# Performance work log

Hardware: AMD Instinct MI355X
Metric: run time of the kernel (lower is better)

The kernel has to match this reference:

```python
import jax, jax.numpy as jnp
import numpy as np

B, S, D, R = 4, 4096, 1024, 128
EPS_MAG = 1e-8
EPS_LN = 1e-5


def setup_inputs() -> dict:
    key = jax.random.key(0)
    ks = jax.random.split(key, 24)
    w = lambda k, shape, s=0.02: (jax.random.normal(k, shape, jnp.float32) * s)
    d = {}
    d["x"] = jax.random.normal(ks[0], (B, S, D), jnp.float32)
    d["W_dt_down"] = w(ks[1], (D, R))            # dt_proj_down (no bias)
    d["W_dt_up"] = w(ks[2], (R, D))
    d["b_dt_up"] = jnp.full((D,), -4.0, jnp.float32)  # nn.init.constant_(-4.0)
    d["W_gate"] = w(ks[3], (D, D)); d["b_gate"] = jnp.zeros((D,), jnp.float32)
    d["W_phi1"] = w(ks[4], (D, D)); d["b_phi1"] = jnp.zeros((D,), jnp.float32)
    d["W_phi2"] = w(ks[5], (D, D)); d["b_phi2"] = jnp.zeros((D,), jnp.float32)
    d["omega_base"] = jax.random.normal(ks[6], (D,), jnp.float32) * 0.1
    d["W_omega"] = w(ks[7], (D, D)); d["b_omega"] = jnp.zeros((D,), jnp.float32)
    d["W_mag"] = w(ks[8], (D, D)); d["b_mag"] = jnp.zeros((D,), jnp.float32)
    d["W_qoff"] = w(ks[9], (D, D)); d["b_qoff"] = jnp.zeros((D,), jnp.float32)
    d["ln_g"] = jnp.ones((2 * D,), jnp.float32); d["ln_b"] = jnp.zeros((2 * D,), jnp.float32)
    d["W_out1"] = w(ks[10], (2 * D, D)); d["b_out1"] = jnp.zeros((D,), jnp.float32)
    d["W_out2"] = w(ks[11], (D, D)); d["b_out2"] = jnp.zeros((D,), jnp.float32)
    return d


def _forward(x, W_dt_down, W_dt_up, b_dt_up, W_gate, b_gate, W_phi1, b_phi1,
             W_phi2, b_phi2, omega_base, W_omega, b_omega, W_mag, b_mag,
             W_qoff, b_qoff, ln_g, ln_b, W_out1, b_out1, W_out2, b_out2):
    h = x  # expand_factor == 1 -> in_proj is Identity
    # input-dependent delta (low-rank)
    dt = jax.nn.softplus((h @ W_dt_down) @ W_dt_up + b_dt_up)        # [B,S,D]
    select_gate = jax.nn.sigmoid(h @ W_gate + b_gate)
    omega = omega_base + (h @ W_omega + b_omega)
    omega_scaled = omega * dt * 0.01
    phi_init = jax.nn.gelu(h @ W_phi1 + b_phi1, approximate=False) @ W_phi2 + b_phi2
    phi = phi_init + jnp.cumsum(omega_scaled, axis=1)                # phase accumulation
    magnitude = jax.nn.sigmoid(h @ W_mag + b_mag) * 5.0
    content = select_gate * h * magnitude
    memory_real = jnp.cumsum(content * jnp.cos(phi), axis=1)
    memory_imag = jnp.cumsum(content * jnp.sin(phi), axis=1)
    acc_mag = jnp.cumsum(magnitude * select_gate, axis=1)
    sqrt_mag = jnp.sqrt(acc_mag + EPS_MAG)
    mr = memory_real / sqrt_mag
    mi = memory_imag / sqrt_mag
    # rotation-based retrieval
    phi_q = phi + (h @ W_qoff + b_qoff)
    cq, sq = jnp.cos(phi_q), jnp.sin(phi_q)
    retrieved_real = mr * cq + mi * sq
    retrieved_imag = mi * cq - mr * sq
    ctx = jnp.concatenate([retrieved_real, retrieved_imag], axis=-1)  # [B,S,2D]
    mu = jnp.mean(ctx, axis=-1, keepdims=True)
    var = jnp.mean((ctx - mu) ** 2, axis=-1, keepdims=True)
    ln = (ctx - mu) / jnp.sqrt(var + EPS_LN) * ln_g + ln_b
    out = jax.nn.gelu(ln @ W_out1 + b_out1, approximate=False) @ W_out2 + b_out2
    return x + out


def reference(x, W_dt_down, W_dt_up, b_dt_up, W_gate, b_gate, W_phi1, b_phi1,
              W_phi2, b_phi2, omega_base, W_omega, b_omega, W_mag, b_mag,
              W_qoff, b_qoff, ln_g, ln_b, W_out1, b_out1, W_out2, b_out2):
    return _forward(x, W_dt_down, W_dt_up, b_dt_up, W_gate, b_gate, W_phi1, b_phi1,
                    W_phi2, b_phi2, omega_base, W_omega, b_omega, W_mag, b_mag,
                    W_qoff, b_qoff, ln_g, ln_b, W_out1, b_out1, W_out2, b_out2)
```

## Files before the change

kernel.cpp:

```cpp
#include <hip/hip_runtime.h>


#define D_ 1024
#define S_ 4096
#define MQ 4096
#define MF 16384
#define CHUNK 64
#define NCH (S_/CHUNK)

typedef float f32x4 __attribute__((ext_vector_type(4)));
typedef __bf16 bf16x8 __attribute__((ext_vector_type(8)));
typedef short s16x8 __attribute__((ext_vector_type(8)));

typedef __attribute__((address_space(1))) void gvoid;
typedef __attribute__((address_space(3))) void lvoid;

__device__ __forceinline__ void g2l16(const void* g, void* l) {
  __builtin_amdgcn_global_load_lds((gvoid*)g, (lvoid*)l, 16, 0, 0);
}

__device__ __forceinline__ float bflo(unsigned int w){ union{unsigned int i; float f;} c; c.i = w<<16; return c.f; }
__device__ __forceinline__ float bfhi(unsigned int w){ union{unsigned int i; float f;} c; c.i = w & 0xFFFF0000u; return c.f; }
__device__ __forceinline__ unsigned short f2bf(float f){
  union{float f; unsigned int i;} c; c.f=f;
  unsigned int u = c.i + 0x7FFFu + ((c.i>>16)&1u);
  return (unsigned short)(u>>16);
}
__device__ __forceinline__ unsigned int pack2(float lo, float hi){
  return (unsigned int)f2bf(lo) | ((unsigned int)f2bf(hi)<<16);
}

__device__ __forceinline__ float sig_(float x){ return 1.f/(1.f+__expf(-x)); }
__device__ __forceinline__ float gelu_(float x){ return 0.5f*x*(1.f+erff(x*0.70710678118654752440f)); }
__device__ __forceinline__ float softplus_(float x){ return (x>0.f) ? x + log1pf(__expf(-x)) : log1pf(__expf(x)); }

template<int MODE>
__global__ __launch_bounds__(256)
void gemmF(const unsigned short* __restrict__ A0,
           const unsigned short* __restrict__ A1,
           const unsigned short* __restrict__ B0,
           const unsigned short* __restrict__ B1,
           const float* __restrict__ bias0,
           const float* __restrict__ bias1,
           const float* __restrict__ extra,
           unsigned short* __restrict__ out0,
           unsigned short* __restrict__ out1,
           float* __restrict__ outf)
{
  __shared__ unsigned short As[2][128*32];
  __shared__ unsigned short Bs[2][128*32];
  const int tid = threadIdx.x;
  const int m0 = blockIdx.x * 128;
  const int n0 = blockIdx.y * 128;
  const int lane = tid & 63;
  const int wv = tid >> 6;
  const int wr = wv >> 1, wc = wv & 1;
  const int fr = lane & 15, fg = lane >> 4;

  const int r0 = tid >> 2;
  const int r1 = (tid + 256) >> 2;
  const int k8 = (tid & 3) * 8;

  const unsigned short* Ap; const unsigned short* Bp;
  int lda, ldb, K, brow0;
  if constexpr (MODE == 0)      { Ap=A0; lda=1024; K=1024; Bp=B0; ldb=1024; brow0=n0; }
  else if constexpr (MODE == 2) { Ap=A0; lda=2048; K=2048; Bp=B0; ldb=2048; brow0=n0; }
  else if constexpr (MODE == 3) { Ap=A0; lda=1024; K=1024; Bp=B0; ldb=1024; brow0=n0; }
  else {
    if (n0 < 1024) { Ap=A0; lda=1024; K=1024; Bp=B0; ldb=1024; brow0=n0; }
    else           { Ap=A1; lda=128;  K=128;  Bp=B1; ldb=128;  brow0=n0-1024; }
  }

  const unsigned short* ArowA = Ap + (size_t)(m0+r0)*lda + k8;
  const unsigned short* ArowB = Ap + (size_t)(m0+r1)*lda + k8;
  const unsigned short* BrowA = Bp + (size_t)(brow0+r0)*ldb + k8;
  const unsigned short* BrowB = Bp + (size_t)(brow0+r1)*ldb + k8;

  f32x4 acc[4][4];
#pragma unroll
  for (int i=0;i<4;i++)
#pragma unroll
    for (int j=0;j<4;j++)
#pragma unroll
      for (int q=0;q<4;q++) acc[i][j][q] = 0.f;

  auto STAGE = [&](int buf, int t) {
    const int k0 = t << 5;
    g2l16(ArowA + k0, &As[buf][(size_t)tid*8]);
    g2l16(ArowB + k0, &As[buf][(size_t)(tid+256)*8]);
    g2l16(BrowA + k0, &Bs[buf][(size_t)tid*8]);
    g2l16(BrowB + k0, &Bs[buf][(size_t)(tid+256)*8]);
  };
  auto COMPUTE = [&](int buf) {
    s16x8 af[4], bfr[4];
#pragma unroll
    for (int mf=0; mf<4; mf++) af[mf]  = *(const s16x8*)&As[buf][(wr*64 + mf*16 + fr)*32 + fg*8];
#pragma unroll
    for (int nf=0; nf<4; nf++) bfr[nf] = *(const s16x8*)&Bs[buf][(wc*64 + nf*16 + fr)*32 + fg*8];
#pragma unroll
    for (int mf=0; mf<4; mf++)
#pragma unroll
      for (int nf=0; nf<4; nf++)
        acc[mf][nf] = __builtin_amdgcn_mfma_f32_16x16x32_bf16(
          __builtin_bit_cast(bf16x8, af[mf]), __builtin_bit_cast(bf16x8, bfr[nf]),
          acc[mf][nf], 0, 0, 0);
  };

  const int nt = K >> 5;
  STAGE(0, 0);
  STAGE(1, 1);
  int cur = 0;
  for (int t = 0; t < nt - 1; ++t) {
    asm volatile("s_waitcnt vmcnt(4)" ::: "memory");
    __builtin_amdgcn_s_barrier();
    __builtin_amdgcn_sched_barrier(0);
    COMPUTE(cur);
    __builtin_amdgcn_s_barrier();
    __builtin_amdgcn_sched_barrier(0);
    if (t + 2 < nt) STAGE(cur, t + 2);
    cur ^= 1;
  }
  asm volatile("s_waitcnt vmcnt(0)" ::: "memory");
  __builtin_amdgcn_s_barrier();
  __builtin_amdgcn_sched_barrier(0);
  COMPUTE(cur);

  const int slice = n0 >> 10;
#pragma unroll
  for (int mf=0; mf<4; mf++) {
#pragma unroll
    for (int nf=0; nf<4; nf++) {
      const int gn = n0 + wc*64 + nf*16 + fr;
      float bv;
      if constexpr (MODE == 1) bv = (n0 < 1024) ? bias0[gn] : bias1[gn-1024];
      else bv = bias0[gn];
#pragma unroll
      for (int q=0; q<4; q++) {
        const int gm = m0 + wr*64 + mf*16 + fg*4 + q;
        const float z = acc[mf][nf][q] + bv;
        if constexpr (MODE == 0) {
          if (slice < 5) {
            const float r = (slice==0) ? sig_(z)
                          : (slice==2) ? gelu_(z)
                          : (slice==3) ? sig_(z)*5.f : z;
            out0[(size_t)slice*MQ*1024 + (size_t)gm*1024 + (gn&1023)] = f2bf(r);
          } else {
            out1[(size_t)gm*128 + (gn-5120)] = f2bf(z);
          }
        } else if constexpr (MODE == 1) {
          if (slice == 0) out0[(size_t)gm*1024 + gn] = f2bf(z);
          else            out1[(size_t)gm*1024 + (gn-1024)] = f2bf(softplus_(z));
        } else if constexpr (MODE == 2) {
          out0[(size_t)gm*1024 + gn] = f2bf(gelu_(z));
        } else {
          const size_t idx = (size_t)gm*1024 + gn;
          outf[idx] = z + extra[idx];
        }
      }
    }
  }
}

__global__ __launch_bounds__(256)
void cvtx_k(const float* __restrict__ x, unsigned int* __restrict__ hb)
{
  const size_t i = (size_t)blockIdx.x*256 + threadIdx.x;
  const float4 v = *(const float4*)(x + i*4);
  hb[i*2]   = pack2(v.x, v.y);
  hb[i*2+1] = pack2(v.z, v.w);
}

__global__ __launch_bounds__(256)
void tconv_k(const float* __restrict__ W, unsigned short* __restrict__ Wt, int K, int N)
{
  __shared__ float tile[32][33];
  const int kb = blockIdx.x*32, nb = blockIdx.y*32;
  const int tx = threadIdx.x & 31, ty = threadIdx.x >> 5;
#pragma unroll
  for (int i=0;i<32;i+=8) tile[ty+i][tx] = W[(size_t)(kb+ty+i)*N + (nb+tx)];
  __syncthreads();
#pragma unroll
  for (int i=0;i<32;i+=8) Wt[(size_t)(nb+ty+i)*K + (kb+tx)] = f2bf(tile[tx][ty+i]);
}

struct P7 { const float* s[7]; unsigned short* d[7]; };
__global__ __launch_bounds__(256)
void tconv7_k(P7 p)
{
  __shared__ float tile[32][33];
  const float* W = p.s[blockIdx.z];
  unsigned short* Wt = p.d[blockIdx.z];
  const int kb = blockIdx.x*32, nb = blockIdx.y*32;
  const int tx = threadIdx.x & 31, ty = threadIdx.x >> 5;
#pragma unroll
  for (int i=0;i<32;i+=8) tile[ty+i][tx] = W[(size_t)(kb+ty+i)*1024 + (nb+tx)];
  __syncthreads();
#pragma unroll
  for (int i=0;i<32;i+=8) Wt[(size_t)(nb+ty+i)*1024 + (kb+tx)] = f2bf(tile[tx][ty+i]);
}

__global__ __launch_bounds__(256)
void biascat_k(const float* bg, const float* bo, const float* ob, const float* bp1,
               const float* bm, const float* bq, float* bc)
{
  const int i = blockIdx.x*256 + threadIdx.x;
  if (i >= 5248) return;
  const int s = i >> 10, d = i & 1023;
  float v;
  if (s==0) v = bg[d];
  else if (s==1) v = bo[d] + ob[d];
  else if (s==2) v = bp1[d];
  else if (s==3) v = bm[d];
  else if (s==4) v = bq[d];
  else v = 0.f;
  bc[i] = v;
}

__global__ __launch_bounds__(256)
void scan1_k(unsigned int* __restrict__ zgate, unsigned int* __restrict__ zmag,
             unsigned int* __restrict__ zomega, const unsigned int* __restrict__ zdt,
             const unsigned int* __restrict__ hb,
             float* __restrict__ sumPhi, float* __restrict__ sumGm)
{
  const int flat = blockIdx.x*256 + threadIdx.x;
  const int dh = flat & 511;
  const int bc = flat >> 9;
  size_t i = (size_t)bc*CHUNK*(D_/2) + dh;
  float sp0=0,sp1=0,sg0=0,sg1=0;
  for (int s=0;s<CHUNK;s++,i+=D_/2) {
    const unsigned ga=zgate[i], mg=zmag[i], om=zomega[i], dt=zdt[i], hh=hb[i];
    const float ga0=bflo(ga), ga1=bfhi(ga), mg0=bflo(mg), mg1=bfhi(mg);
    const float od0 = bflo(om)*bflo(dt)*0.01f, od1 = bfhi(om)*bfhi(dt)*0.01f;
    const unsigned odp = pack2(od0, od1);
    zomega[i] = odp;
    sp0 += bflo(odp); sp1 += bfhi(odp);
    const float g0 = ga0*mg0, g1 = ga1*mg1;
    const unsigned gmp = pack2(g0, g1);
    zmag[i] = gmp;
    sg0 += bflo(gmp); sg1 += bfhi(gmp);
    zgate[i] = pack2(g0*bflo(hh), g1*bfhi(hh));
  }
  const int sidx = bc*D_ + dh*2;
  sumPhi[sidx]=sp0; sumPhi[sidx+1]=sp1;
  sumGm[sidx]=sg0;  sumGm[sidx+1]=sg1;
}

__global__ __launch_bounds__(256)
void scan2_k(float* __restrict__ a, float* __restrict__ b)
{
  const int chain = (blockIdx.x*256 + threadIdx.x) >> 6;
  const int lane  = threadIdx.x & 63;
  const size_t i = (size_t)lane*D_ + chain;
  const float v = a[i], w = b[i];
  float vi = v, wi = w;
#pragma unroll
  for (int off=1; off<64; off<<=1) {
    const float t = __shfl_up(vi, off, 64);
    const float u = __shfl_up(wi, off, 64);
    if (lane >= off) { vi += t; wi += u; }
  }
  a[i] = vi - v;
  b[i] = wi - w;
}

__global__ __launch_bounds__(256)
void scan3_k(const unsigned int* __restrict__ omdt, const unsigned int* __restrict__ content,
             const unsigned int* __restrict__ phinit, const float* __restrict__ phiOff,
             float* __restrict__ sumRe, float* __restrict__ sumIm)
{
  const int flat = blockIdx.x*256 + threadIdx.x;
  const int dh = flat & 511;
  const int bc = flat >> 9;
  size_t i = (size_t)bc*CHUNK*(D_/2) + dh;
  const int sidx = bc*D_ + dh*2;
  float p0 = phiOff[sidx], p1 = phiOff[sidx+1];
  float re0=0,re1=0,im0=0,im1=0;
  for (int s=0;s<CHUNK;s++,i+=D_/2) {
    const unsigned od = omdt[i], ct = content[i], pi = phinit[i];
    p0 += bflo(od); p1 += bfhi(od);
    const float phi0 = bflo(pi)+p0, phi1 = bfhi(pi)+p1;
    float s0,c0,s1,c1;
    __sincosf(phi0,&s0,&c0);
    __sincosf(phi1,&s1,&c1);
    const float ct0=bflo(ct), ct1=bfhi(ct);
    re0 += ct0*c0; im0 += ct0*s0;
    re1 += ct1*c1; im1 += ct1*s1;
  }
  sumRe[sidx]=re0; sumRe[sidx+1]=re1;
  sumIm[sidx]=im0; sumIm[sidx+1]=im1;
}

__global__ __launch_bounds__(256)
void scan5_k(const unsigned int* __restrict__ omdt, const unsigned int* __restrict__ content,
             const unsigned int* __restrict__ phinit, const unsigned int* __restrict__ gm,
             const unsigned int* __restrict__ qoff,
             const float* __restrict__ phiOff, const float* __restrict__ gmOff,
             const float* __restrict__ reOff, const float* __restrict__ imOff,
             unsigned int* __restrict__ ctx)
{
  const int flat = blockIdx.x*256 + threadIdx.x;
  const int dh = flat & 511;
  const int bc = flat >> 9;
  size_t i = (size_t)bc*CHUNK*(D_/2) + dh;
  const int sidx = bc*D_ + dh*2;
  float p0 = phiOff[sidx], p1 = phiOff[sidx+1];
  float ag0 = gmOff[sidx], ag1 = gmOff[sidx+1];
  float re0 = reOff[sidx], re1 = reOff[sidx+1];
  float im0 = imOff[sidx], im1 = imOff[sidx+1];
  const int mtok0 = bc*CHUNK;
  for (int s=0;s<CHUNK;s++,i+=D_/2) {
    const unsigned od = omdt[i], ct = content[i], pi = phinit[i], gq = gm[i], qo = qoff[i];
    p0 += bflo(od); p1 += bfhi(od);
    const float phi0 = bflo(pi)+p0, phi1 = bfhi(pi)+p1;
    float sn0,cs0,sn1,cs1;
    __sincosf(phi0,&sn0,&cs0);
    __sincosf(phi1,&sn1,&cs1);
    const float ct0=bflo(ct), ct1=bfhi(ct);
    re0 += ct0*cs0; im0 += ct0*sn0;
    re1 += ct1*cs1; im1 += ct1*sn1;
    ag0 += bflo(gq); ag1 += bfhi(gq);
    const float inv0 = rsqrtf(ag0 + 1e-8f), inv1 = rsqrtf(ag1 + 1e-8f);
    const float mr0 = re0*inv0, mi0 = im0*inv0;
    const float mr1 = re1*inv1, mi1 = im1*inv1;
    const float pq0 = phi0 + bflo(qo), pq1 = phi1 + bfhi(qo);
    float sq0,cq0,sq1,cq1;
    __sincosf(pq0,&sq0,&cq0);
    __sincosf(pq1,&sq1,&cq1);
    const size_t cb = (size_t)(mtok0+s)*D_ + dh;
    ctx[cb]        = pack2(mr0*cq0 + mi0*sq0, mr1*cq1 + mi1*sq1);
    ctx[cb + D_/2] = pack2(mi0*cq0 - mr0*sq0, mi1*cq1 - mr1*sq1);
  }
}

__global__ __launch_bounds__(256)
void ln_k(unsigned int* __restrict__ ctx, const float* __restrict__ gam, const float* __restrict__ bet)
{
  const int m = blockIdx.x, tid = threadIdx.x;
  const size_t base = (size_t)m*1024 + tid*4;
  const uint4 t = *(const uint4*)(ctx + base);
  float v[8] = { bflo(t.x), bfhi(t.x), bflo(t.y), bfhi(t.y),
                 bflo(t.z), bfhi(t.z), bflo(t.w), bfhi(t.w) };
  float s=0.f, ss=0.f;
#pragma unroll
  for (int j=0;j<8;j++){ s+=v[j]; ss+=v[j]*v[j]; }
  for (int o=32;o;o>>=1){ s += __shfl_xor(s,o); ss += __shfl_xor(ss,o); }
  __shared__ float red[8];
  const int wv = tid>>6, lane = tid&63;
  if (lane==0){ red[wv]=s; red[4+wv]=ss; }
  __syncthreads();
  s  = red[0]+red[1]+red[2]+red[3];
  ss = red[4]+red[5]+red[6]+red[7];
  const float mu = s*(1.f/2048.f);
  const float rstd = rsqrtf(ss*(1.f/2048.f) - mu*mu + 1e-5f);
  const int col = tid*8;
  float o[8];
#pragma unroll
  for (int j=0;j<8;j++) o[j] = (v[j]-mu)*rstd*gam[col+j] + bet[col+j];
  uint4 w;
  w.x = pack2(o[0],o[1]); w.y = pack2(o[2],o[3]);
  w.z = pack2(o[4],o[5]); w.w = pack2(o[6],o[7]);
  *(uint4*)(ctx + base) = w;
}

extern "C" void kernel_launch(void* const* d_in, const int* in_sizes, int n_in,
                              void* d_out, int out_size, void* d_ws, size_t ws_size,
                              hipStream_t stream)
{
  const float* x     = (const float*)d_in[0];
  const float* Wdd   = (const float*)d_in[1];
  const float* Wdu   = (const float*)d_in[2];
  const float* bdu   = (const float*)d_in[3];
  const float* Wg    = (const float*)d_in[4];
  const float* bg    = (const float*)d_in[5];
  const float* Wp1   = (const float*)d_in[6];
  const float* bp1   = (const float*)d_in[7];
  const float* Wp2   = (const float*)d_in[8];
  const float* bp2   = (const float*)d_in[9];
  const float* obase = (const float*)d_in[10];
  const float* Wo    = (const float*)d_in[11];
  const float* bo    = (const float*)d_in[12];
  const float* Wm    = (const float*)d_in[13];
  const float* bm    = (const float*)d_in[14];
  const float* Wq    = (const float*)d_in[15];
  const float* bq    = (const float*)d_in[16];
  const float* lng   = (const float*)d_in[17];
  const float* lnb   = (const float*)d_in[18];
  const float* Wo1   = (const float*)d_in[19];
  const float* bo1   = (const float*)d_in[20];
  const float* Wo2   = (const float*)d_in[21];
  const float* bo2   = (const float*)d_in[22];

  char* basep = (char*)d_ws;
  size_t off = 0;
  auto alloc = [&](size_t n) { char* q = basep + off; off = (off + n + 255) & ~(size_t)255; return q; };

  unsigned short* ctxF = (unsigned short*)alloc((size_t)MF*2048*2);
  char* qbase = alloc((size_t)5*MQ*1024*2 + (size_t)2*MQ*1024*2
                      + (size_t)MQ*1024*2 + (size_t)MQ*128*2);
  unsigned short* cat1 = (unsigned short*)qbase;
  unsigned short* cat2 = cat1 + (size_t)5*MQ*1024;
  unsigned short* hb   = cat2 + (size_t)2*MQ*1024;
  unsigned short* t1   = hb   + (size_t)MQ*1024;
  unsigned short* a3   = (unsigned short*)qbase;
  unsigned short* wt_cat = (unsigned short*)alloc((size_t)5248*1024*2);
  unsigned short* wt_p2  = (unsigned short*)alloc(1024*1024*2);
  unsigned short* wt_du  = (unsigned short*)alloc(1024*128*2);
  unsigned short* wt_o1  = (unsigned short*)alloc((size_t)1024*2048*2);
  unsigned short* wt_o2  = (unsigned short*)alloc(1024*1024*2);
  float* bias_cat = (float*)alloc(5248*4);
  float* sumPhi = (float*)alloc((size_t)NCH*D_*4);
  float* sumGm  = (float*)alloc((size_t)NCH*D_*4);
  float* sumRe  = (float*)alloc((size_t)NCH*D_*4);
  float* sumIm  = (float*)alloc((size_t)NCH*D_*4);

  const dim3 blk(256);

  P7 p7;
  p7.s[0]=Wg;  p7.d[0]=wt_cat + (size_t)0*1024*1024;
  p7.s[1]=Wo;  p7.d[1]=wt_cat + (size_t)1*1024*1024;
  p7.s[2]=Wp1; p7.d[2]=wt_cat + (size_t)2*1024*1024;
  p7.s[3]=Wm;  p7.d[3]=wt_cat + (size_t)3*1024*1024;
  p7.s[4]=Wq;  p7.d[4]=wt_cat + (size_t)4*1024*1024;
  p7.s[5]=Wp2; p7.d[5]=wt_p2;
  p7.s[6]=Wo2; p7.d[6]=wt_o2;
  tconv7_k<<<dim3(32,32,7), blk, 0, stream>>>(p7);
  tconv_k<<<dim3(32,4),  blk, 0, stream>>>(Wdd, wt_cat + (size_t)5120*1024, 1024,128);
  tconv_k<<<dim3(4,32),  blk, 0, stream>>>(Wdu, wt_du, 128,1024);
  tconv_k<<<dim3(64,32), blk, 0, stream>>>(Wo1, wt_o1, 2048,1024);
  biascat_k<<<21, blk, 0, stream>>>(bg, bo, obase, bp1, bm, bq, bias_cat);

  unsigned short* zgate  = cat1;
  unsigned short* zomega = cat1 + (size_t)1*MQ*1024;
  unsigned short* zphi1  = cat1 + (size_t)2*MQ*1024;
  unsigned short* zmag   = cat1 + (size_t)3*MQ*1024;
  unsigned short* zqoff  = cat1 + (size_t)4*MQ*1024;
  unsigned short* zpin   = cat2;
  unsigned short* zdt    = cat2 + (size_t)1*MQ*1024;

  for (int q = 0; q < 4; q++) {
    const float* xq = x + (size_t)q*MQ*D_;

    cvtx_k<<<MQ*D_/1024, blk, 0, stream>>>(xq, (unsigned int*)hb);

    gemmF<0><<<dim3(MQ/128, 41), blk, 0, stream>>>(hb, nullptr, wt_cat, nullptr,
                                                   bias_cat, nullptr, nullptr,
                                                   cat1, t1, nullptr);
    gemmF<1><<<dim3(MQ/128, 16), blk, 0, stream>>>(zphi1, t1, wt_p2, wt_du,
                                                   bp2, bdu, nullptr,
                                                   zpin, zdt, nullptr);
    scan1_k<<<128, blk, 0, stream>>>((unsigned int*)zgate,(unsigned int*)zmag,(unsigned int*)zomega,
                                     (const unsigned int*)zdt,(const unsigned int*)hb, sumPhi, sumGm);
    scan2_k<<<256, blk, 0, stream>>>(sumPhi, sumGm);
    scan3_k<<<128, blk, 0, stream>>>((const unsigned int*)zomega,(const unsigned int*)zgate,
                                     (const unsigned int*)zpin, sumPhi, sumRe, sumIm);
    scan2_k<<<256, blk, 0, stream>>>(sumRe, sumIm);
    scan5_k<<<128, blk, 0, stream>>>((const unsigned int*)zomega,(const unsigned int*)zgate,
                                     (const unsigned int*)zpin,(const unsigned int*)zmag,
                                     (const unsigned int*)zqoff,
                                     sumPhi, sumGm, sumRe, sumIm,
                                     (unsigned int*)ctxF + (size_t)q*MQ*1024);
  }

  ln_k<<<MF, blk, 0, stream>>>((unsigned int*)ctxF, lng, lnb);
  gemmF<2><<<dim3(MF/128, 8), blk, 0, stream>>>(ctxF, nullptr, wt_o1, nullptr,
                                                bo1, nullptr, nullptr,
                                                a3, nullptr, nullptr);
  gemmF<3><<<dim3(MF/128, 8), blk, 0, stream>>>(a3, nullptr, wt_o2, nullptr,
                                                bo2, nullptr, x,
                                                nullptr, nullptr, (float*)d_out);
}
```

Before: 918.2 us.

## Fold low-rank dt projection into fused weight and process two halves

```diff
diff --git a/kernel.cpp b/kernel.cpp
--- a/kernel.cpp
+++ b/kernel.cpp
@@ -3,10 +3,8 @@
 
 #define D_ 1024
 #define S_ 4096
-#define MQ 4096
-#define MF 16384
+#define MH 8192
 #define CHUNK 64
-#define NCH (S_/CHUNK)
 
 typedef float f32x4 __attribute__((ext_vector_type(4)));
 typedef __bf16 bf16x8 __attribute__((ext_vector_type(8)));
@@ -34,17 +32,13 @@
 __device__ __forceinline__ float gelu_(float x){ return 0.5f*x*(1.f+erff(x*0.70710678118654752440f)); }
 __device__ __forceinline__ float softplus_(float x){ return (x>0.f) ? x + log1pf(__expf(-x)) : log1pf(__expf(x)); }
 
-template<int MODE>
-__global__ __launch_bounds__(256)
-void gemmF(const unsigned short* __restrict__ A0,
-           const unsigned short* __restrict__ A1,
-           const unsigned short* __restrict__ B0,
-           const unsigned short* __restrict__ B1,
-           const float* __restrict__ bias0,
-           const float* __restrict__ bias1,
+template<int EPI, int KK>
+__global__ __launch_bounds__(256)
+void gemmH(const unsigned short* __restrict__ A,
+           const unsigned short* __restrict__ Bt,
+           const float* __restrict__ bias,
            const float* __restrict__ extra,
            unsigned short* __restrict__ out0,
-           unsigned short* __restrict__ out1,
            float* __restrict__ outf)
 {
   __shared__ unsigned short As[2][128*32];
@@ -58,23 +52,12 @@
   const int fr = lane & 15, fg = lane >> 4;
 
   const int r0 = tid >> 2;
-  const int r1 = (tid + 256) >> 2;
   const int k8 = (tid & 3) * 8;
 
-  const unsigned short* Ap; const unsigned short* Bp;
-  int lda, ldb, K, brow0;
-  if constexpr (MODE == 0)      { Ap=A0; lda=1024; K=1024; Bp=B0; ldb=1024; brow0=n0; }
-  else if constexpr (MODE == 2) { Ap=A0; lda=2048; K=2048; Bp=B0; ldb=2048; brow0=n0; }
-  else if constexpr (MODE == 3) { Ap=A0; lda=1024; K=1024; Bp=B0; ldb=1024; brow0=n0; }
-  else {
-    if (n0 < 1024) { Ap=A0; lda=1024; K=1024; Bp=B0; ldb=1024; brow0=n0; }
-    else           { Ap=A1; lda=128;  K=128;  Bp=B1; ldb=128;  brow0=n0-1024; }
-  }
-
-  const unsigned short* ArowA = Ap + (size_t)(m0+r0)*lda + k8;
-  const unsigned short* ArowB = Ap + (size_t)(m0+r1)*lda + k8;
-  const unsigned short* BrowA = Bp + (size_t)(brow0+r0)*ldb + k8;
-  const unsigned short* BrowB = Bp + (size_t)(brow0+r1)*ldb + k8;
+  const unsigned short* ArowA = A  + (size_t)(m0+r0)*KK + k8;
+  const unsigned short* ArowB = A  + (size_t)(m0+r0+64)*KK + k8;
+  const unsigned short* BrowA = Bt + (size_t)(n0+r0)*KK + k8;
+  const unsigned short* BrowB = Bt + (size_t)(n0+r0+64)*KK + k8;
 
   f32x4 acc[4][4];
 #pragma unroll
@@ -106,7 +89,7 @@
           acc[mf][nf], 0, 0, 0);
   };
 
-  const int nt = K >> 5;
+  const int nt = KK >> 5;
   STAGE(0, 0);
   STAGE(1, 1);
   int cur = 0;
@@ -131,30 +114,27 @@
 #pragma unroll
     for (int nf=0; nf<4; nf++) {
       const int gn = n0 + wc*64 + nf*16 + fr;
-      float bv;
-      if constexpr (MODE == 1) bv = (n0 < 1024) ? bias0[gn] : bias1[gn-1024];
-      else bv = bias0[gn];
+      float bv = 0.f;
+      if constexpr (EPI != 4) bv = bias[gn];
 #pragma unroll
       for (int q=0; q<4; q++) {
         const int gm = m0 + wr*64 + mf*16 + fg*4 + q;
         const float z = acc[mf][nf][q] + bv;
-        if constexpr (MODE == 0) {
-          if (slice < 5) {
-            const float r = (slice==0) ? sig_(z)
-                          : (slice==2) ? gelu_(z)
-                          : (slice==3) ? sig_(z)*5.f : z;
-            out0[(size_t)slice*MQ*1024 + (size_t)gm*1024 + (gn&1023)] = f2bf(r);
-          } else {
-            out1[(size_t)gm*128 + (gn-5120)] = f2bf(z);
-          }
-        } else if constexpr (MODE == 1) {
-          if (slice == 0) out0[(size_t)gm*1024 + gn] = f2bf(z);
-          else            out1[(size_t)gm*1024 + (gn-1024)] = f2bf(softplus_(z));
-        } else if constexpr (MODE == 2) {
+        if constexpr (EPI == 0) {
+          const float r = (slice==1) ? sig_(z)*5.f
+                        : (slice==3) ? sig_(z)
+                        : (slice==4) ? softplus_(z)
+                        : (slice==5) ? gelu_(z) : z;
+          out0[(size_t)slice*((size_t)MH*1024) + (size_t)gm*1024 + (gn & 1023)] = f2bf(r);
+        } else if constexpr (EPI == 1) {
+          out0[(size_t)gm*1024 + gn] = f2bf(z);
+        } else if constexpr (EPI == 2) {
           out0[(size_t)gm*1024 + gn] = f2bf(gelu_(z));
-        } else {
+        } else if constexpr (EPI == 3) {
           const size_t idx = (size_t)gm*1024 + gn;
           outf[idx] = z + extra[idx];
+        } else {
+          out0[(size_t)gm*1024 + gn] = f2bf(z);
         }
       }
     }
@@ -200,19 +180,19 @@
 }
 
 __global__ __launch_bounds__(256)
-void biascat_k(const float* bg, const float* bo, const float* ob, const float* bp1,
-               const float* bm, const float* bq, float* bc)
+void biascat_k(const float* bo, const float* ob, const float* bm, const float* bq,
+               const float* bg, const float* bdu, const float* bp1, float* bc)
 {
   const int i = blockIdx.x*256 + threadIdx.x;
-  if (i >= 5248) return;
+  if (i >= 6144) return;
   const int s = i >> 10, d = i & 1023;
   float v;
-  if (s==0) v = bg[d];
-  else if (s==1) v = bo[d] + ob[d];
-  else if (s==2) v = bp1[d];
-  else if (s==3) v = bm[d];
-  else if (s==4) v = bq[d];
-  else v = 0.f;
+  if (s==0) v = bo[d] + ob[d];
+  else if (s==1) v = bm[d];
+  else if (s==2) v = bq[d];
+  else if (s==3) v = bg[d];
+  else if (s==4) v = bdu[d];
+  else v = bp1[d];
   bc[i] = v;
 }
 
@@ -250,7 +230,8 @@
 {
   const int chain = (blockIdx.x*256 + threadIdx.x) >> 6;
   const int lane  = threadIdx.x & 63;
-  const size_t i = (size_t)lane*D_ + chain;
+  const int bb = chain >> 10, d = chain & 1023;
+  const size_t i = (size_t)(bb*64 + lane)*D_ + d;
   const float v = a[i], w = b[i];
   float vi = v, wi = w;
 #pragma unroll
@@ -394,78 +375,73 @@
   size_t off = 0;
   auto alloc = [&](size_t n) { char* q = basep + off; off = (off + n + 255) & ~(size_t)255; return q; };
 
-  unsigned short* ctxF = (unsigned short*)alloc((size_t)MF*2048*2);
-  char* qbase = alloc((size_t)5*MQ*1024*2 + (size_t)2*MQ*1024*2
-                      + (size_t)MQ*1024*2 + (size_t)MQ*128*2);
-  unsigned short* cat1 = (unsigned short*)qbase;
-  unsigned short* cat2 = cat1 + (size_t)5*MQ*1024;
-  unsigned short* hb   = cat2 + (size_t)2*MQ*1024;
-  unsigned short* t1   = hb   + (size_t)MQ*1024;
-  unsigned short* a3   = (unsigned short*)qbase;
-  unsigned short* wt_cat = (unsigned short*)alloc((size_t)5248*1024*2);
+  const size_t S = (size_t)MH*1024;
+  unsigned short* cat1 = (unsigned short*)alloc(7*S*2);
+  unsigned short* zomega = cat1 + 0*S;
+  unsigned short* zmag   = cat1 + 1*S;
+  unsigned short* zqoff  = cat1 + 2*S;
+  unsigned short* zgate  = cat1 + 3*S;
+  unsigned short* zdt    = cat1 + 4*S;
+  unsigned short* zphi1  = cat1 + 5*S;
+  unsigned short* hb     = cat1 + 6*S;
+  unsigned short* ctx    = zphi1;
+  unsigned short* a3     = cat1;
+  unsigned short* zpin   = (unsigned short*)alloc(S*2);
+  unsigned short* wt_cat = (unsigned short*)alloc((size_t)6144*1024*2);
   unsigned short* wt_p2  = (unsigned short*)alloc(1024*1024*2);
   unsigned short* wt_du  = (unsigned short*)alloc(1024*128*2);
+  unsigned short* wddb   = (unsigned short*)alloc(1024*128*2);
   unsigned short* wt_o1  = (unsigned short*)alloc((size_t)1024*2048*2);
   unsigned short* wt_o2  = (unsigned short*)alloc(1024*1024*2);
-  float* bias_cat = (float*)alloc(5248*4);
-  float* sumPhi = (float*)alloc((size_t)NCH*D_*4);
-  float* sumGm  = (float*)alloc((size_t)NCH*D_*4);
-  float* sumRe  = (float*)alloc((size_t)NCH*D_*4);
-  float* sumIm  = (float*)alloc((size_t)NCH*D_*4);
+  float* bias_cat = (float*)alloc(6144*4);
+  float* sumPhi = (float*)alloc((size_t)128*D_*4);
+  float* sumGm  = (float*)alloc((size_t)128*D_*4);
+  float* sumRe  = (float*)alloc((size_t)128*D_*4);
+  float* sumIm  = (float*)alloc((size_t)128*D_*4);
 
   const dim3 blk(256);
 
   P7 p7;
-  p7.s[0]=Wg;  p7.d[0]=wt_cat + (size_t)0*1024*1024;
-  p7.s[1]=Wo;  p7.d[1]=wt_cat + (size_t)1*1024*1024;
-  p7.s[2]=Wp1; p7.d[2]=wt_cat + (size_t)2*1024*1024;
-  p7.s[3]=Wm;  p7.d[3]=wt_cat + (size_t)3*1024*1024;
-  p7.s[4]=Wq;  p7.d[4]=wt_cat + (size_t)4*1024*1024;
+  p7.s[0]=Wo;  p7.d[0]=wt_cat + (size_t)0*1024*1024;
+  p7.s[1]=Wm;  p7.d[1]=wt_cat + (size_t)1*1024*1024;
+  p7.s[2]=Wq;  p7.d[2]=wt_cat + (size_t)2*1024*1024;
+  p7.s[3]=Wg;  p7.d[3]=wt_cat + (size_t)3*1024*1024;
+  p7.s[4]=Wp1; p7.d[4]=wt_cat + (size_t)5*1024*1024;
   p7.s[5]=Wp2; p7.d[5]=wt_p2;
   p7.s[6]=Wo2; p7.d[6]=wt_o2;
   tconv7_k<<<dim3(32,32,7), blk, 0, stream>>>(p7);
-  tconv_k<<<dim3(32,4),  blk, 0, stream>>>(Wdd, wt_cat + (size_t)5120*1024, 1024,128);
   tconv_k<<<dim3(4,32),  blk, 0, stream>>>(Wdu, wt_du, 128,1024);
   tconv_k<<<dim3(64,32), blk, 0, stream>>>(Wo1, wt_o1, 2048,1024);
-  biascat_k<<<21, blk, 0, stream>>>(bg, bo, obase, bp1, bm, bq, bias_cat);
-
-  unsigned short* zgate  = cat1;
-  unsigned short* zomega = cat1 + (size_t)1*MQ*1024;
-  unsigned short* zphi1  = cat1 + (size_t)2*MQ*1024;
-  unsigned short* zmag   = cat1 + (size_t)3*MQ*1024;
-  unsigned short* zqoff  = cat1 + (size_t)4*MQ*1024;
-  unsigned short* zpin   = cat2;
-  unsigned short* zdt    = cat2 + (size_t)1*MQ*1024;
-
-  for (int q = 0; q < 4; q++) {
-    const float* xq = x + (size_t)q*MQ*D_;
-
-    cvtx_k<<<MQ*D_/1024, blk, 0, stream>>>(xq, (unsigned int*)hb);
-
-    gemmF<0><<<dim3(MQ/128, 41), blk, 0, stream>>>(hb, nullptr, wt_cat, nullptr,
-                                                   bias_cat, nullptr, nullptr,
-                                                   cat1, t1, nullptr);
-    gemmF<1><<<dim3(MQ/128, 16), blk, 0, stream>>>(zphi1, t1, wt_p2, wt_du,
-                                                   bp2, bdu, nullptr,
-                                                   zpin, zdt, nullptr);
-    scan1_k<<<128, blk, 0, stream>>>((unsigned int*)zgate,(unsigned int*)zmag,(unsigned int*)zomega,
+  cvtx_k<<<128, blk, 0, stream>>>(Wdd, (unsigned int*)wddb);
+  gemmH<4,128><<<dim3(8,8), blk, 0, stream>>>(wt_du, wddb, nullptr, nullptr,
+                                              wt_cat + (size_t)4*1024*1024, nullptr);
+  biascat_k<<<24, blk, 0, stream>>>(bo, obase, bm, bq, bg, bdu, bp1, bias_cat);
+
+  for (int h = 0; h < 2; h++) {
+    const float* xh = x + (size_t)h*MH*D_;
+    float* outh     = (float*)d_out + (size_t)h*MH*D_;
+
+    cvtx_k<<<MH*D_/1024, blk, 0, stream>>>(xh, (unsigned int*)hb);
+
+    gemmH<0,1024><<<dim3(MH/128, 48), blk, 0, stream>>>(hb, wt_cat, bias_cat,
+                                                        nullptr, cat1, nullptr);
+    gemmH<1,1024><<<dim3(MH/128, 8), blk, 0, stream>>>(zphi1, wt_p2, bp2,
+                                                       nullptr, zpin, nullptr);
+    scan1_k<<<256, blk, 0, stream>>>((unsigned int*)zgate,(unsigned int*)zmag,(unsigned int*)zomega,
                                      (const unsigned int*)zdt,(const unsigned int*)hb, sumPhi, sumGm);
-    scan2_k<<<256, blk, 0, stream>>>(sumPhi, sumGm);
-    scan3_k<<<128, blk, 0, stream>>>((const unsigned int*)zomega,(const unsigned int*)zgate,
+    scan2_k<<<512, blk, 0, stream>>>(sumPhi, sumGm);
+    scan3_k<<<256, blk, 0, stream>>>((const unsigned int*)zomega,(const unsigned int*)zgate,
                                      (const unsigned int*)zpin, sumPhi, sumRe, sumIm);
-    scan2_k<<<256, blk, 0, stream>>>(sumRe, sumIm);
-    scan5_k<<<128, blk, 0, stream>>>((const unsigned int*)zomega,(const unsigned int*)zgate,
+    scan2_k<<<512, blk, 0, stream>>>(sumRe, sumIm);
+    scan5_k<<<256, blk, 0, stream>>>((const unsigned int*)zomega,(const unsigned int*)zgate,
                                      (const unsigned int*)zpin,(const unsigned int*)zmag,
                                      (const unsigned int*)zqoff,
-                                     sumPhi, sumGm, sumRe, sumIm,
-                                     (unsigned int*)ctxF + (size_t)q*MQ*1024);
-  }
-
-  ln_k<<<MF, blk, 0, stream>>>((unsigned int*)ctxF, lng, lnb);
-  gemmF<2><<<dim3(MF/128, 8), blk, 0, stream>>>(ctxF, nullptr, wt_o1, nullptr,
-                                                bo1, nullptr, nullptr,
-                                                a3, nullptr, nullptr);
-  gemmF<3><<<dim3(MF/128, 8), blk, 0, stream>>>(a3, nullptr, wt_o2, nullptr,
-                                                bo2, nullptr, x,
-                                                nullptr, nullptr, (float*)d_out);
-}
+                                     sumPhi, sumGm, sumRe, sumIm, (unsigned int*)ctx);
+
+    ln_k<<<MH, blk, 0, stream>>>((unsigned int*)ctx, lng, lnb);
+    gemmH<2,2048><<<dim3(MH/128, 8), blk, 0, stream>>>(ctx, wt_o1, bo1,
+                                                       nullptr, a3, nullptr);
+    gemmH<3,1024><<<dim3(MH/128, 8), blk, 0, stream>>>(a3, wt_o2, bo2,
+                                                       xh, nullptr, outh);
+  }
+}
```

Measured after the change: 829.8 us, median of 3. 9.6% less time.
